# Kernel optimization log

Hardware: AMD Instinct MI355X
Metric: run time of the kernel (lower is better)

The kernel has to match this reference:

```python
import jax, jax.numpy as jnp
import numpy as np

MARGIN = 1.0
SAFE_RADIUS = 4.0
B, C, H, W = 16, 48, 64, 64
N_CORR = 2048


def _normalize(x, eps=1e-12):
    # F.normalize(x, dim=0): L2-normalize over the channel axis
    return x / jnp.maximum(jnp.linalg.norm(x, axis=0, keepdims=True), eps)


def _grid_positions(h, w):
    i, j = jnp.meshgrid(jnp.arange(h, dtype=jnp.float32),
                        jnp.arange(w, dtype=jnp.float32), indexing='ij')
    return jnp.stack([i.reshape(-1), j.reshape(-1)], axis=0)


def _per_image(df1, df2, att1, att2, ids, fp2):
    c, h1, w1 = df1.shape
    _, h2, w2 = df2.shape
    all_d1 = _normalize(df1.reshape(c, -1))   # [c, h1*w1]
    all_d2 = _normalize(df2.reshape(c, -1))   # [c, h2*w2]

    d1 = all_d1[:, ids]                       # [c, n] gathered anchors
    s1 = att1.reshape(-1)[ids]                # [n]
    d2 = _normalize(df2[:, fp2[0], fp2[1]])   # [c, n] gathered positives

    positive_distance = 2.0 - 2.0 * jnp.sum(d1 * d2, axis=0)  # [n]

    # hard-negative mining in image 2
    grid2 = _grid_positions(h2, w2)           # [2, h2*w2]
    pd2 = jnp.max(jnp.abs(fp2.astype(jnp.float32)[:, :, None] - grid2[:, None, :]), axis=0)
    out2 = (pd2 > SAFE_RADIUS).astype(df1.dtype)            # [n, h2*w2]
    dm2 = 2.0 - 2.0 * jnp.einsum('cn,cm->nm', d1, all_d2)   # [n, h2*w2]
    neg2 = jnp.min(dm2 + (1.0 - out2) * 10.0, axis=1)       # [n]

    # hard-negative mining in image 1
    grid1 = _grid_positions(h1, w1)
    fp1 = grid1[:, ids]                                      # [2, n]
    pd1 = jnp.max(jnp.abs(fp1[:, :, None] - grid1[:, None, :]), axis=0)
    out1 = (pd1 > SAFE_RADIUS).astype(df1.dtype)
    dm1 = 2.0 - 2.0 * jnp.einsum('cn,cm->nm', d2, all_d1)
    neg1 = jnp.min(dm1 + (1.0 - out1) * 10.0, axis=1)

    diff = positive_distance - jnp.minimum(neg1, neg2)
    s2 = att2[0, fp2[0], fp2[1]]
    w = s1 * s2
    return jnp.sum(w * jax.nn.relu(MARGIN + diff)) / jnp.sum(w)


def setup_inputs() -> dict:
    key = jax.random.key(0)
    k1, k2, k3, k4, k5, k6 = jax.random.split(key, 6)
    return {
        'x1_encoded': jax.random.normal(k1, (B, C, H, W), dtype=jnp.float32),
        'x2_encoded': jax.random.normal(k2, (B, C, H, W), dtype=jnp.float32),
        'attentions1': jax.random.uniform(k3, (B, 1, H, W), dtype=jnp.float32),
        'attentions2': jax.random.uniform(k4, (B, 1, H, W), dtype=jnp.float32),
        'ids': jax.random.randint(k5, (B, N_CORR), 0, H * W),
        'fmap_pos2': jax.random.randint(k6, (B, 2, N_CORR), 0, H),
    }


def reference(x1_encoded, x2_encoded, attentions1, attentions2, ids, fmap_pos2):
    per_image = jax.vmap(_per_image)(x1_encoded, x2_encoded, attentions1,
                                     attentions2, ids, fmap_pos2)
    return jnp.mean(per_image).reshape(1)
```

## Files before the change

### kernel.cpp

```cpp
#include <hip/hip_runtime.h>
#include <stdint.h>

#define BB 16
#define HW 4096
#define NC 2048
#define KHW 72
#define KB 144

typedef __attribute__((ext_vector_type(8))) __bf16 bf16x8;
typedef __attribute__((ext_vector_type(8))) short short8;
typedef __attribute__((ext_vector_type(4))) float floatx4;

static __device__ __forceinline__ unsigned short f2bf(float f) {
    unsigned u = __builtin_bit_cast(unsigned, f);
    unsigned r = u + 0x7fffu + ((u >> 16) & 1u);
    return (unsigned short)(r >> 16);
}

#define GLD16(g, l) __builtin_amdgcn_global_load_lds((const __attribute__((address_space(1))) void*)(g), (__attribute__((address_space(3))) void*)(l), 16, 0, 0)
#define GLD4(g, l)  __builtin_amdgcn_global_load_lds((const __attribute__((address_space(1))) void*)(g), (__attribute__((address_space(3))) void*)(l), 4, 0, 0)

__global__ void prep_fused(const float* __restrict__ x1, const float* __restrict__ x2,
                           const int* __restrict__ ids, const int* __restrict__ fp2,
                           unsigned short* __restrict__ dbp,
                           int* __restrict__ perm, int* __restrict__ qcol_s,
                           int* __restrict__ aqpack, unsigned int* __restrict__ maxs2enc) {
    __shared__ __align__(16) unsigned char slab[36864 + 4096 + 1024];
    int bid = blockIdx.x, tid = threadIdx.x;
    if (bid < 512) {
        int img = bid >> 8;
        int b = (bid >> 4) & 15;
        int p0 = (bid & 15) * 256;
        int w = tid >> 6, l = tid & 63;
        const float* x = img ? x2 : x1;
        const float* base = x + ((size_t)b * 48 + w * 12) * HW + p0 + 4 * l;
        floatx4 v[12];
        floatx4 ps = {0.f, 0.f, 0.f, 0.f};
#pragma unroll
        for (int cc = 0; cc < 12; ++cc) {
            v[cc] = *(const floatx4*)(base + cc * HW);
#pragma unroll
            for (int q = 0; q < 4; ++q) ps[q] = fmaf(v[cc][q], v[cc][q], ps[q]);
        }
        float* psum = (float*)(slab + 36864);
        float* rbuf = (float*)(slab + 36864 + 4096);
        *(floatx4*)(psum + w * 256 + 4 * l) = ps;
        __syncthreads();
        float s = psum[tid] + psum[256 + tid] + psum[512 + tid] + psum[768 + tid];
        rbuf[tid] = 1.f / fmaxf(sqrtf(s), 1e-12f);
        __syncthreads();
        floatx4 rv = *(const floatx4*)(rbuf + 4 * l);
#pragma unroll
        for (int q = 0; q < 4; ++q) {
            unsigned u[6];
#pragma unroll
            for (int p = 0; p < 6; ++p) {
                u[p] = (unsigned)f2bf(v[2 * p][q] * rv[q]) |
                       ((unsigned)f2bf(v[2 * p + 1][q] * rv[q]) << 16);
            }
            unsigned char* dst = slab + (4 * l + q) * KB + w * 24;
            *(uint2*)(dst + 0)  = make_uint2(u[0], u[1]);
            *(uint2*)(dst + 8)  = make_uint2(u[2], u[3]);
            *(uint2*)(dst + 16) = make_uint2(u[4], u[5]);
        }
        uint4 z4 = {0u, 0u, 0u, 0u};
#pragma unroll
        for (int z = 0; z < 3; ++z)
            *(uint4*)(slab + tid * KB + 96 + z * 16) = z4;
        __syncthreads();
        unsigned char* dstb = (unsigned char*)dbp + ((size_t)(img * BB + b) * HW + p0) * KB;
#pragma unroll
        for (int rr = 0; rr < 9; ++rr) {
            int idx = rr * 4096 + tid * 16;
            *(floatx4*)(dstb + idx) = *(const floatx4*)(slab + idx);
        }
    } else if (bid < 544) {
        int* hist = (int*)slab;
        int* base = hist + 64;
        int seg = bid - 512;
        int dir = seg >> 4, b = seg & 15;
        if (tid < 64) hist[tid] = 0;
        __syncthreads();
#pragma unroll
        for (int k = 0; k < 8; ++k) {
            int n = k * 256 + tid;
            int idv = ids[b * NC + n];
            int i2 = fp2[b * 2 * NC + n];
            int qi = (dir == 0) ? i2 : (idv >> 6);
            atomicAdd(&hist[qi], 1);
        }
        __syncthreads();
        if (tid == 0) {
            int run = 0;
            for (int k = 0; k < 64; ++k) { base[k] = run; run += hist[k]; }
        }
        __syncthreads();
#pragma unroll
        for (int k = 0; k < 8; ++k) {
            int n = k * 256 + tid;
            int idv = ids[b * NC + n];
            int i2 = fp2[b * 2 * NC + n];
            int j2 = fp2[b * 2 * NC + NC + n];
            int qi, qj, qcol;
            if (dir == 0) { qi = i2; qj = j2; qcol = idv; }
            else          { qi = idv >> 6; qj = idv & 63; qcol = i2 * 64 + j2; }
            int slot = atomicAdd(&base[qi], 1);
            perm[seg * NC + slot] = n;
            qcol_s[seg * NC + slot] = qcol;
            aqpack[seg * NC + slot] = (qi << 8) | qj;
        }
    } else {
        int t = (bid - 544) * 256 + tid;
        uint4* p = (uint4*)maxs2enc;
        uint4 z = {0u, 0u, 0u, 0u};
#pragma unroll
        for (int k = 0; k < 8; ++k) p[k * 2048 + t] = z;
    }
}

static __device__ __forceinline__ void dma_tile(const unsigned char* g, unsigned char* l,
                                                int wave, int lane) {
#pragma unroll
    for (int rr = 0; rr < 4; ++rr)
        GLD16(g + rr * 4096 + wave * 1024 + lane * 16, l + rr * 4096 + wave * 1024);
#pragma unroll
    for (int rr = 0; rr < 2; ++rr)
        GLD4(g + 16384 + rr * 1024 + wave * 256 + lane * 4, l + 16384 + rr * 1024 + wave * 256);
}

template <int DIR>
__device__ __forceinline__ void maxscore_core(
    const unsigned short* __restrict__ dbp,
    const int* __restrict__ perm, const int* __restrict__ qcol_s,
    const int* __restrict__ aqpack, unsigned int* __restrict__ maxs2enc) {
    __shared__ __align__(16) unsigned char smem[36864];

    int tid = threadIdx.x, wave = tid >> 6, lane = tid & 63;
    int quad = lane >> 4, cl = lane & 15;
    int gid = blockIdx.x;
    int b = gid & 15;
    int mtile = (gid >> 4) & 15, nq = gid >> 8;
    int seg = DIR * BB + b;
    int qbase = mtile * 128;
    int dbimg = 1 - DIR;

    const unsigned char* dbQ = (const unsigned char*)(dbp + (size_t)(DIR * BB + b) * HW * KHW);
    short8 afr[2][2];
#pragma unroll
    for (int t = 0; t < 2; ++t) {
        int slot = qbase + wave * 32 + t * 16 + cl;
        int qc = qcol_s[seg * NC + slot];
        const unsigned char* src = dbQ + (size_t)qc * KB;
        afr[t][0] = *(const short8*)(src + quad * 16);
        afr[t][1] = *(const short8*)(src + 64 + quad * 16);
    }
    float qif[2][4], qjc[2][4];
    float cl_f = (float)cl;
#pragma unroll
    for (int t = 0; t < 2; ++t)
#pragma unroll
        for (int r = 0; r < 4; ++r) {
            int slot = qbase + wave * 32 + t * 16 + quad * 4 + r;
            int ap = aqpack[seg * NC + slot];
            qif[t][r] = (float)(ap >> 8);
            qjc[t][r] = (float)(ap & 255) - cl_f;
        }
    int wb = seg * NC + qbase + wave * 32;
    int qimin = __builtin_amdgcn_readfirstlane(aqpack[wb] >> 8);
    int qimax = __builtin_amdgcn_readfirstlane(aqpack[wb + 31] >> 8);

    const unsigned char* dsrc =
        (const unsigned char*)(dbp + ((size_t)(dbimg * BB + b) * HW + nq * 1024) * KHW);
    dma_tile(dsrc, smem, wave, lane);

    const floatx4 zf = {0.f, 0.f, 0.f, 0.f};
    float mx[2][4];
#pragma unroll
    for (int t = 0; t < 2; ++t)
#pragma unroll
        for (int r = 0; r < 4; ++r) mx[t][r] = -1e30f;

    for (int tile = 0; tile < 8; ++tile) {
        unsigned char* buf = smem + (tile & 1) * 18432;
        __syncthreads();
        if (tile + 1 < 8)
            dma_tile(dsrc + (tile + 1) * 18432, smem + ((tile + 1) & 1) * 18432, wave, lane);
        int mi0 = (nq * 1024 + tile * 128) >> 6;
#pragma unroll
        for (int half = 0; half < 2; ++half) {
            int mi = mi0 + half;
            bool active = (mi >= qimin - 4) && (mi <= qimax + 4);
            if (active) {
                float mi_f = (float)mi;
                float qjd[2][4];
#pragma unroll
                for (int t = 0; t < 2; ++t)
#pragma unroll
                    for (int r = 0; r < 4; ++r) {
                        bool rowblk = fabsf(qif[t][r] - mi_f) <= 4.0f;
                        qjd[t][r] = rowblk ? qjc[t][r] : 1e9f;
                    }
#pragma unroll
                for (int js = 0; js < 4; ++js) {
                    int sub = half * 4 + js;
                    float jj = (float)(js * 16);
                    short8 b0 = *(const short8*)(buf + (sub * 16 + cl) * KB + quad * 16);
                    short8 b1 = *(const short8*)(buf + (sub * 16 + cl) * KB + 64 + quad * 16);
#pragma unroll
                    for (int t = 0; t < 2; ++t) {
                        floatx4 acc = __builtin_amdgcn_mfma_f32_16x16x32_bf16(
                            __builtin_bit_cast(bf16x8, afr[t][0]),
                            __builtin_bit_cast(bf16x8, b0), zf, 0, 0, 0);
                        acc = __builtin_amdgcn_mfma_f32_16x16x32_bf16(
                            __builtin_bit_cast(bf16x8, afr[t][1]),
                            __builtin_bit_cast(bf16x8, b1), acc, 0, 0, 0);
#pragma unroll
                        for (int r = 0; r < 4; ++r) {
                            bool ok = fabsf(qjd[t][r] - jj) > 4.0f;
                            mx[t][r] = ok ? fmaxf(mx[t][r], acc[r]) : mx[t][r];
                        }
                    }
                }
            } else {
#pragma unroll
                for (int js = 0; js < 4; ++js) {
                    int sub = half * 4 + js;
                    short8 b0 = *(const short8*)(buf + (sub * 16 + cl) * KB + quad * 16);
                    short8 b1 = *(const short8*)(buf + (sub * 16 + cl) * KB + 64 + quad * 16);
#pragma unroll
                    for (int t = 0; t < 2; ++t) {
                        floatx4 acc = __builtin_amdgcn_mfma_f32_16x16x32_bf16(
                            __builtin_bit_cast(bf16x8, afr[t][0]),
                            __builtin_bit_cast(bf16x8, b0), zf, 0, 0, 0);
                        acc = __builtin_amdgcn_mfma_f32_16x16x32_bf16(
                            __builtin_bit_cast(bf16x8, afr[t][1]),
                            __builtin_bit_cast(bf16x8, b1), acc, 0, 0, 0);
#pragma unroll
                        for (int r = 0; r < 4; ++r)
                            mx[t][r] = fmaxf(mx[t][r], acc[r]);
                    }
                }
            }
        }
    }

#pragma unroll
    for (int t = 0; t < 2; ++t)
#pragma unroll
        for (int r = 0; r < 4; ++r) {
            float v = mx[t][r];
            v = fmaxf(v, __shfl_xor(v, 1, 16));
            v = fmaxf(v, __shfl_xor(v, 2, 16));
            v = fmaxf(v, __shfl_xor(v, 4, 16));
            v = fmaxf(v, __shfl_xor(v, 8, 16));
            mx[t][r] = v;
        }
    if (cl == 0) {
#pragma unroll
        for (int t = 0; t < 2; ++t)
#pragma unroll
            for (int r = 0; r < 4; ++r) {
                int slot = qbase + wave * 32 + t * 16 + quad * 4 + r;
                int orig = perm[seg * NC + slot];
                float v = mx[t][r] + 2.0f;
                atomicMax(&maxs2enc[(size_t)seg * NC + orig],
                          __builtin_bit_cast(unsigned, v));
            }
    }
}

__global__ __launch_bounds__(256, 4) void maxscore_d0(
    const unsigned short* __restrict__ dbp, const int* __restrict__ perm,
    const int* __restrict__ qcol_s, const int* __restrict__ aqpack,
    unsigned int* __restrict__ maxs2enc) {
    maxscore_core<0>(dbp, perm, qcol_s, aqpack, maxs2enc);
}
__global__ __launch_bounds__(256, 4) void maxscore_d1(
    const unsigned short* __restrict__ dbp, const int* __restrict__ perm,
    const int* __restrict__ qcol_s, const int* __restrict__ aqpack,
    unsigned int* __restrict__ maxs2enc) {
    maxscore_core<1>(dbp, perm, qcol_s, aqpack, maxs2enc);
}

__global__ void loss_kernel(const float* __restrict__ att1, const float* __restrict__ att2,
                            const int* __restrict__ ids, const int* __restrict__ fp2,
                            const unsigned short* __restrict__ dbp,
                            const unsigned int* __restrict__ maxs2enc,
                            float* __restrict__ pnum, float* __restrict__ pden) {
    int b = blockIdx.x >> 3, chunk = blockIdx.x & 7;
    int tid = threadIdx.x;
    int n = chunk * 256 + tid;
    int idv = ids[b * NC + n];
    int i2 = fp2[b * 2 * NC + n], j2 = fp2[b * 2 * NC + NC + n];
    const uint4* a4 = (const uint4*)(dbp + ((size_t)(0 * BB + b) * HW + idv) * KHW);
    const uint4* b4 = (const uint4*)(dbp + ((size_t)(1 * BB + b) * HW + i2 * 64 + j2) * KHW);
    float dot = 0.f;
#pragma unroll
    for (int i = 0; i < 6; ++i) {
        uint4 xa = a4[i], xb = b4[i];
        const unsigned* xu = (const unsigned*)&xa;
        const unsigned* yu = (const unsigned*)&xb;
#pragma unroll
        for (int w = 0; w < 4; ++w) {
            float xl = __builtin_bit_cast(float, xu[w] << 16);
            float xh = __builtin_bit_cast(float, xu[w] & 0xffff0000u);
            float yl = __builtin_bit_cast(float, yu[w] << 16);
            float yh = __builtin_bit_cast(float, yu[w] & 0xffff0000u);
            dot = fmaf(xl, yl, fmaf(xh, yh, dot));
        }
    }
    float m0 = __builtin_bit_cast(float, maxs2enc[(size_t)(0 * BB + b) * NC + n]) - 2.0f;
    float m1 = __builtin_bit_cast(float, maxs2enc[(size_t)(1 * BB + b) * NC + n]) - 2.0f;
    float ms = fmaxf(m0, m1);
    float diff = (2.f - 2.f * dot) - (2.f - 2.f * ms);
    float w = att1[b * HW + idv] * att2[b * HW + i2 * 64 + j2];
    float num = w * fmaxf(0.f, 1.f + diff);
    float den = w;
    __shared__ float sn[256], sd[256];
    sn[tid] = num; sd[tid] = den;
    __syncthreads();
    for (int s = 128; s > 0; s >>= 1) {
        if (tid < s) { sn[tid] += sn[tid + s]; sd[tid] += sd[tid + s]; }
        __syncthreads();
    }
    if (tid == 0) { pnum[blockIdx.x] = sn[0]; pden[blockIdx.x] = sd[0]; }
}

__global__ void final_kernel(const float* __restrict__ pnum, const float* __restrict__ pden,
                             float* __restrict__ out) {
    int tid = threadIdx.x;
    __shared__ float r[16];
    if (tid < 16) {
        float n = 0.f, d = 0.f;
#pragma unroll
        for (int c = 0; c < 8; ++c) { n += pnum[tid * 8 + c]; d += pden[tid * 8 + c]; }
        r[tid] = n / d;
    }
    __syncthreads();
    if (tid == 0) {
        float s = 0.f;
#pragma unroll
        for (int k = 0; k < 16; ++k) s += r[k];
        out[0] = s * (1.f / BB);
    }
}

extern "C" void kernel_launch(void* const* d_in, const int* in_sizes, int n_in,
                              void* d_out, int out_size, void* d_ws, size_t ws_size,
                              hipStream_t stream) {
    const float* x1  = (const float*)d_in[0];
    const float* x2  = (const float*)d_in[1];
    const float* att1 = (const float*)d_in[2];
    const float* att2 = (const float*)d_in[3];
    const int* ids   = (const int*)d_in[4];
    const int* fp2   = (const int*)d_in[5];
    float* out = (float*)d_out;

    unsigned char* w = (unsigned char*)d_ws;
    unsigned short* dbp = (unsigned short*)(w + 0);
    int* perm    = (int*)(w + 18874368);
    int* qcol_s  = (int*)(w + 19136512);
    int* aqpack  = (int*)(w + 19398656);
    unsigned int* maxs2enc = (unsigned int*)(w + 19660800);
    float* pnum  = (float*)(w + 19922944);
    float* pden  = (float*)(w + 19923456);

    prep_fused<<<dim3(552), dim3(256), 0, stream>>>(x1, x2, ids, fp2, dbp,
                                                    perm, qcol_s, aqpack, maxs2enc);
    maxscore_d0<<<dim3(1024), dim3(256), 0, stream>>>(dbp, perm, qcol_s, aqpack, maxs2enc);
    maxscore_d1<<<dim3(1024), dim3(256), 0, stream>>>(dbp, perm, qcol_s, aqpack, maxs2enc);
    loss_kernel<<<dim3(128), dim3(256), 0, stream>>>(att1, att2, ids, fp2, dbp, maxs2enc, pnum, pden);
    final_kernel<<<dim3(1), dim3(64), 0, stream>>>(pnum, pden, out);
}
```

Before: 136.7 us.

## Merge direction kernels, enlarge query tile, replace atomics with per-slice max buffer

Combines the two per-direction maxscore kernels into one launch that covers both directions. Each block now handles 256 queries instead of 128 (4 fragments per wave), so every database tile loaded into LDS is reused by twice as many queries, and the grid is split into 4 database quarters. Per-quarter maxima are written directly to a slice buffer, which removes the atomicMax and the zero-initialisation blocks; the loss kernel then reduces over the 8 slices. The cost is more registers per wave (launch bounds no longer request 4 blocks per SM), a larger workspace, and a wider active-row window per wave, which may reduce the row-skip pruning.

```diff
diff --git a/kernel.cpp b/kernel.cpp
--- a/kernel.cpp
+++ b/kernel.cpp
@@ -24,7 +24,7 @@
                            const int* __restrict__ ids, const int* __restrict__ fp2,
                            unsigned short* __restrict__ dbp,
                            int* __restrict__ perm, int* __restrict__ qcol_s,
-                           int* __restrict__ aqpack, unsigned int* __restrict__ maxs2enc) {
+                           int* __restrict__ aqpack) {
     __shared__ __align__(16) unsigned char slab[36864 + 4096 + 1024];
     int bid = blockIdx.x, tid = threadIdx.x;
     if (bid < 512) {
@@ -74,7 +74,7 @@
             int idx = rr * 4096 + tid * 16;
             *(floatx4*)(dstb + idx) = *(const floatx4*)(slab + idx);
         }
-    } else if (bid < 544) {
+    } else {
         int* hist = (int*)slab;
         int* base = hist + 64;
         int seg = bid - 512;
@@ -109,12 +109,6 @@
             qcol_s[seg * NC + slot] = qcol;
             aqpack[seg * NC + slot] = (qi << 8) | qj;
         }
-    } else {
-        int t = (bid - 544) * 256 + tid;
-        uint4* p = (uint4*)maxs2enc;
-        uint4 z = {0u, 0u, 0u, 0u};
-#pragma unroll
-        for (int k = 0; k < 8; ++k) p[k * 2048 + t] = z;
     }
 }
 
@@ -128,55 +122,53 @@
         GLD4(g + 16384 + rr * 1024 + wave * 256 + lane * 4, l + 16384 + rr * 1024 + wave * 256);
 }
 
-template <int DIR>
-__device__ __forceinline__ void maxscore_core(
+__global__ __launch_bounds__(256) void maxscore_mfma(
     const unsigned short* __restrict__ dbp,
     const int* __restrict__ perm, const int* __restrict__ qcol_s,
-    const int* __restrict__ aqpack, unsigned int* __restrict__ maxs2enc) {
+    const int* __restrict__ aqpack, float* __restrict__ maxs2) {
     __shared__ __align__(16) unsigned char smem[36864];
 
     int tid = threadIdx.x, wave = tid >> 6, lane = tid & 63;
     int quad = lane >> 4, cl = lane & 15;
     int gid = blockIdx.x;
-    int b = gid & 15;
-    int mtile = (gid >> 4) & 15, nq = gid >> 8;
-    int seg = DIR * BB + b;
-    int qbase = mtile * 128;
-    int dbimg = 1 - DIR;
-
-    const unsigned char* dbQ = (const unsigned char*)(dbp + (size_t)(DIR * BB + b) * HW * KHW);
-    short8 afr[2][2];
-#pragma unroll
-    for (int t = 0; t < 2; ++t) {
-        int slot = qbase + wave * 32 + t * 16 + cl;
+    int seg = gid & 31, dir = seg >> 4, b = seg & 15;
+    int rest = gid >> 5, mtile = rest & 7, nq = rest >> 3;
+    int qbase = mtile * 256;
+    int dbimg = 1 - dir;
+
+    const unsigned char* dbQ = (const unsigned char*)(dbp + (size_t)(dir * BB + b) * HW * KHW);
+    short8 afr[4][2];
+#pragma unroll
+    for (int t = 0; t < 4; ++t) {
+        int slot = qbase + wave * 64 + t * 16 + cl;
         int qc = qcol_s[seg * NC + slot];
         const unsigned char* src = dbQ + (size_t)qc * KB;
         afr[t][0] = *(const short8*)(src + quad * 16);
         afr[t][1] = *(const short8*)(src + 64 + quad * 16);
     }
-    float qif[2][4], qjc[2][4];
+    float qif[4][4], qjc[4][4];
     float cl_f = (float)cl;
 #pragma unroll
-    for (int t = 0; t < 2; ++t)
+    for (int t = 0; t < 4; ++t)
 #pragma unroll
         for (int r = 0; r < 4; ++r) {
-            int slot = qbase + wave * 32 + t * 16 + quad * 4 + r;
+            int slot = qbase + wave * 64 + t * 16 + quad * 4 + r;
             int ap = aqpack[seg * NC + slot];
             qif[t][r] = (float)(ap >> 8);
             qjc[t][r] = (float)(ap & 255) - cl_f;
         }
-    int wb = seg * NC + qbase + wave * 32;
+    int wb = seg * NC + qbase + wave * 64;
     int qimin = __builtin_amdgcn_readfirstlane(aqpack[wb] >> 8);
-    int qimax = __builtin_amdgcn_readfirstlane(aqpack[wb + 31] >> 8);
+    int qimax = __builtin_amdgcn_readfirstlane(aqpack[wb + 63] >> 8);
 
     const unsigned char* dsrc =
         (const unsigned char*)(dbp + ((size_t)(dbimg * BB + b) * HW + nq * 1024) * KHW);
     dma_tile(dsrc, smem, wave, lane);
 
     const floatx4 zf = {0.f, 0.f, 0.f, 0.f};
-    float mx[2][4];
-#pragma unroll
-    for (int t = 0; t < 2; ++t)
+    float mx[4][4];
+#pragma unroll
+    for (int t = 0; t < 4; ++t)
 #pragma unroll
         for (int r = 0; r < 4; ++r) mx[t][r] = -1e30f;
 
@@ -192,14 +184,12 @@
             bool active = (mi >= qimin - 4) && (mi <= qimax + 4);
             if (active) {
                 float mi_f = (float)mi;
-                float qjd[2][4];
-#pragma unroll
-                for (int t = 0; t < 2; ++t)
-#pragma unroll
-                    for (int r = 0; r < 4; ++r) {
-                        bool rowblk = fabsf(qif[t][r] - mi_f) <= 4.0f;
-                        qjd[t][r] = rowblk ? qjc[t][r] : 1e9f;
-                    }
+                bool rowok[4][4];
+#pragma unroll
+                for (int t = 0; t < 4; ++t)
+#pragma unroll
+                    for (int r = 0; r < 4; ++r)
+                        rowok[t][r] = fabsf(qif[t][r] - mi_f) > 4.0f;
 #pragma unroll
                 for (int js = 0; js < 4; ++js) {
                     int sub = half * 4 + js;
@@ -207,7 +197,7 @@
                     short8 b0 = *(const short8*)(buf + (sub * 16 + cl) * KB + quad * 16);
                     short8 b1 = *(const short8*)(buf + (sub * 16 + cl) * KB + 64 + quad * 16);
 #pragma unroll
-                    for (int t = 0; t < 2; ++t) {
+                    for (int t = 0; t < 4; ++t) {
                         floatx4 acc = __builtin_amdgcn_mfma_f32_16x16x32_bf16(
                             __builtin_bit_cast(bf16x8, afr[t][0]),
                             __builtin_bit_cast(bf16x8, b0), zf, 0, 0, 0);
@@ -216,7 +206,8 @@
                             __builtin_bit_cast(bf16x8, b1), acc, 0, 0, 0);
 #pragma unroll
                         for (int r = 0; r < 4; ++r) {
-                            bool ok = fabsf(qjd[t][r] - jj) > 4.0f;
+                            float dj = qjc[t][r] - jj;
+                            bool ok = rowok[t][r] || (fabsf(dj) > 4.0f);
                             mx[t][r] = ok ? fmaxf(mx[t][r], acc[r]) : mx[t][r];
                         }
                     }
@@ -228,7 +219,7 @@
                     short8 b0 = *(const short8*)(buf + (sub * 16 + cl) * KB + quad * 16);
                     short8 b1 = *(const short8*)(buf + (sub * 16 + cl) * KB + 64 + quad * 16);
 #pragma unroll
-                    for (int t = 0; t < 2; ++t) {
+                    for (int t = 0; t < 4; ++t) {
                         floatx4 acc = __builtin_amdgcn_mfma_f32_16x16x32_bf16(
                             __builtin_bit_cast(bf16x8, afr[t][0]),
                             __builtin_bit_cast(bf16x8, b0), zf, 0, 0, 0);
@@ -245,7 +236,7 @@
     }
 
 #pragma unroll
-    for (int t = 0; t < 2; ++t)
+    for (int t = 0; t < 4; ++t)
 #pragma unroll
         for (int r = 0; r < 4; ++r) {
             float v = mx[t][r];
@@ -257,35 +248,20 @@
         }
     if (cl == 0) {
 #pragma unroll
-        for (int t = 0; t < 2; ++t)
+        for (int t = 0; t < 4; ++t)
 #pragma unroll
             for (int r = 0; r < 4; ++r) {
-                int slot = qbase + wave * 32 + t * 16 + quad * 4 + r;
+                int slot = qbase + wave * 64 + t * 16 + quad * 4 + r;
                 int orig = perm[seg * NC + slot];
-                float v = mx[t][r] + 2.0f;
-                atomicMax(&maxs2enc[(size_t)seg * NC + orig],
-                          __builtin_bit_cast(unsigned, v));
+                maxs2[((size_t)(nq * 32 + seg)) * NC + orig] = mx[t][r];
             }
     }
-}
-
-__global__ __launch_bounds__(256, 4) void maxscore_d0(
-    const unsigned short* __restrict__ dbp, const int* __restrict__ perm,
-    const int* __restrict__ qcol_s, const int* __restrict__ aqpack,
-    unsigned int* __restrict__ maxs2enc) {
-    maxscore_core<0>(dbp, perm, qcol_s, aqpack, maxs2enc);
-}
-__global__ __launch_bounds__(256, 4) void maxscore_d1(
-    const unsigned short* __restrict__ dbp, const int* __restrict__ perm,
-    const int* __restrict__ qcol_s, const int* __restrict__ aqpack,
-    unsigned int* __restrict__ maxs2enc) {
-    maxscore_core<1>(dbp, perm, qcol_s, aqpack, maxs2enc);
 }
 
 __global__ void loss_kernel(const float* __restrict__ att1, const float* __restrict__ att2,
                             const int* __restrict__ ids, const int* __restrict__ fp2,
                             const unsigned short* __restrict__ dbp,
-                            const unsigned int* __restrict__ maxs2enc,
+                            const float* __restrict__ maxs2,
                             float* __restrict__ pnum, float* __restrict__ pden) {
     int b = blockIdx.x >> 3, chunk = blockIdx.x & 7;
     int tid = threadIdx.x;
@@ -309,9 +285,12 @@
             dot = fmaf(xl, yl, fmaf(xh, yh, dot));
         }
     }
-    float m0 = __builtin_bit_cast(float, maxs2enc[(size_t)(0 * BB + b) * NC + n]) - 2.0f;
-    float m1 = __builtin_bit_cast(float, maxs2enc[(size_t)(1 * BB + b) * NC + n]) - 2.0f;
-    float ms = fmaxf(m0, m1);
+    float ms = -1e30f;
+#pragma unroll
+    for (int s8 = 0; s8 < 8; ++s8) {
+        int slice = (s8 >> 1) * 32 + (s8 & 1) * BB + b;
+        ms = fmaxf(ms, maxs2[(size_t)slice * NC + n]);
+    }
     float diff = (2.f - 2.f * dot) - (2.f - 2.f * ms);
     float w = att1[b * HW + idv] * att2[b * HW + i2 * 64 + j2];
     float num = w * fmaxf(0.f, 1.f + diff);
@@ -361,14 +340,13 @@
     int* perm    = (int*)(w + 18874368);
     int* qcol_s  = (int*)(w + 19136512);
     int* aqpack  = (int*)(w + 19398656);
-    unsigned int* maxs2enc = (unsigned int*)(w + 19660800);
-    float* pnum  = (float*)(w + 19922944);
-    float* pden  = (float*)(w + 19923456);
-
-    prep_fused<<<dim3(552), dim3(256), 0, stream>>>(x1, x2, ids, fp2, dbp,
-                                                    perm, qcol_s, aqpack, maxs2enc);
-    maxscore_d0<<<dim3(1024), dim3(256), 0, stream>>>(dbp, perm, qcol_s, aqpack, maxs2enc);
-    maxscore_d1<<<dim3(1024), dim3(256), 0, stream>>>(dbp, perm, qcol_s, aqpack, maxs2enc);
-    loss_kernel<<<dim3(128), dim3(256), 0, stream>>>(att1, att2, ids, fp2, dbp, maxs2enc, pnum, pden);
+    float* maxs2 = (float*)(w + 19660800);
+    float* pnum  = (float*)(w + 20709376);
+    float* pden  = (float*)(w + 20709888);
+
+    prep_fused<<<dim3(544), dim3(256), 0, stream>>>(x1, x2, ids, fp2, dbp,
+                                                    perm, qcol_s, aqpack);
+    maxscore_mfma<<<dim3(1024), dim3(256), 0, stream>>>(dbp, perm, qcol_s, aqpack, maxs2);
+    loss_kernel<<<dim3(128), dim3(256), 0, stream>>>(att1, att2, ids, fp2, dbp, maxs2, pnum, pden);
     final_kernel<<<dim3(1), dim3(64), 0, stream>>>(pnum, pden, out);
 }
```

Result: slower. 146.3 us (+7.0%).
